# Kernel tuning notes

Measured on AMD Instinct MI355X. Metric: run time of the kernel, lower is better.

The kernel has to match this reference:

```python
import jax, jax.numpy as jnp
import numpy as np

B, S, D_IN, D_OUT = 4, 2048, 2048, 2048
E, R, TOP_K = 8, 8, 2
ALPHA = 16.0
SCALE = ALPHA / R  # alpha / r


def setup_inputs() -> dict:
    key = jax.random.key(0)
    ks = jax.random.split(key, 6)
    x = jax.random.normal(ks[0], (B, S, D_IN), dtype=jnp.float32)
    # base frozen linear: torch Linear weight [out, in], bias [out]
    W_base = jax.random.normal(ks[1], (D_OUT, D_IN), dtype=jnp.float32) / np.sqrt(D_IN)
    b_base = jax.random.normal(ks[2], (D_OUT,), dtype=jnp.float32) * 0.01
    # router: Linear(in_features, num_experts, bias=False) -> weight [E, in]
    W_router = jax.random.normal(ks[3], (E, D_IN), dtype=jnp.float32) / np.sqrt(D_IN)
    # LoRA experts: A [E, r, in], B [E, out, r] (torch inits B to zero; use small
    # random values so outputs/grads are non-trivial -- math is identical)
    A_w = jax.random.normal(ks[4], (E, R, D_IN), dtype=jnp.float32) / np.sqrt(D_IN)
    B_w = jax.random.normal(ks[5], (E, D_OUT, R), dtype=jnp.float32) * 0.02
    return {"x": x, "W_base": W_base, "b_base": b_base,
            "W_router": W_router, "A_w": A_w, "B_w": B_w}


def reference(x, W_base, b_base, W_router, A_w, B_w):
    # frozen base linear: [B,S,out]
    y = jnp.einsum('bsd,od->bso', x, W_base) + b_base
    # router: logits [B,S,E] -> top-k + softmax over the k selected logits
    logits = jnp.einsum('bsd,ed->bse', x, W_router)
    topk_vals, topk_idx = jax.lax.top_k(logits, TOP_K)       # [B,S,k]
    gates = jax.nn.softmax(topk_vals, axis=-1)               # [B,S,k]
    # all-experts LoRA compute (matches the original dense-stack semantics)
    h = jnp.einsum('bsd,erd->bser', x, A_w)                  # [B,S,E,r]
    expert_outs = jnp.einsum('bser,eor->bseo', h, B_w) * SCALE  # [B,S,E,out]
    # gather the top-k expert outputs and combine with gates
    topk_outs = jnp.take_along_axis(expert_outs, topk_idx[..., None], axis=2)  # [B,S,k,out]
    fused = jnp.sum(topk_outs * gates[..., None], axis=2)    # [B,S,out]
    return y + fused
```

## Files before the change

### kernel.cpp

```cpp
#include <hip/hip_runtime.h>

typedef unsigned short u16;
typedef __attribute__((ext_vector_type(8))) short short8;
typedef __attribute__((ext_vector_type(4))) float f32x4;

#define GLL16(g, l) __builtin_amdgcn_global_load_lds(                         \
    (const __attribute__((address_space(1))) void*)(g),                        \
    (__attribute__((address_space(3))) void*)(l), 16, 0, 0)

__device__ __forceinline__ u16 f2bf(float f) {
  union { float f; unsigned u; } v; v.f = f;
  unsigned u = v.u;
  return (u16)((u + 0x7FFFu + ((u >> 16) & 1u)) >> 16);
}

__device__ __forceinline__ float bf2f(u16 u) {
  union { unsigned u; float f; } v; v.u = ((unsigned)u) << 16;
  return v.f;
}

__device__ __forceinline__ ushort4 cvt4(float4 v) {
  ushort4 o; o.x = f2bf(v.x); o.y = f2bf(v.y); o.z = f2bf(v.z); o.w = f2bf(v.w);
  return o;
}

__global__ __launch_bounds__(512) void k_pre(
    const float* __restrict__ x, const float* __restrict__ Wr,
    const float* __restrict__ Wb, const float* __restrict__ Aw,
    const float* __restrict__ Bw,
    u16* __restrict__ xbf, float* __restrict__ logits,
    u16* __restrict__ wbf, u16* __restrict__ aabf, u16* __restrict__ bmt)
{
  __shared__ float wlds[16384];
  {
    const float4* src = (const float4*)Wr;
    float4* dst = (float4*)wlds;
    int t = threadIdx.x;
#pragma unroll
    for (int i = 0; i < 8; ++i) dst[t + i * 512] = src[t + i * 512];
  }
  __syncthreads();
  const int wave = threadIdx.x >> 6, lane = threadIdx.x & 63;
  const float4* wv = (const float4*)wlds;
#pragma unroll 1
  for (int s = 0; s < 2; ++s) {
    int tok = blockIdx.x * 16 + wave * 2 + s;
    const float4* xrow = (const float4*)(x + tok * 2048);
    ushort4* orow = (ushort4*)(xbf + tok * 2048);
    float acc[8];
#pragma unroll
    for (int e = 0; e < 8; ++e) acc[e] = 0.f;
#pragma unroll 1
    for (int i = 0; i < 8; ++i) {
      float4 xv = xrow[lane + i * 64];
      orow[lane + i * 64] = cvt4(xv);
#pragma unroll
      for (int e = 0; e < 8; ++e) {
        float4 b = wv[e * 512 + lane + i * 64];
        acc[e] += xv.x * b.x + xv.y * b.y + xv.z * b.z + xv.w * b.w;
      }
    }
#pragma unroll
    for (int e = 0; e < 8; ++e) {
      float v = acc[e];
#pragma unroll
      for (int off = 32; off > 0; off >>= 1) v += __shfl_xor(v, off, 64);
      acc[e] = v;
    }
    if (lane == 0) {
#pragma unroll
      for (int e = 0; e < 8; ++e) logits[tok * 8 + e] = acc[e];
    }
  }
  const int tidg = blockIdx.x * 512 + threadIdx.x;
  {
    const float4* src = (const float4*)Wb;
    ushort4* dst = (ushort4*)wbf;
#pragma unroll
    for (int i = 0; i < 4; ++i)
      dst[tidg + i * 262144] = cvt4(src[tidg + i * 262144]);
  }
  if (tidg < 32768) {
    ((ushort4*)aabf)[tidg] = cvt4(((const float4*)Aw)[tidg]);
  }
  if (tidg < 2048) {
    const int n = tidg;
#pragma unroll
    for (int e = 0; e < 8; ++e) {
      const float4* src = (const float4*)(Bw + e * 16384 + n * 8);
      ushort4* dst = (ushort4*)(bmt + n * 64 + e * 8);
      dst[0] = cvt4(src[0]);
      dst[1] = cvt4(src[1]);
    }
  }
}

__global__ __launch_bounds__(256) void k_hgemm(
    const u16* __restrict__ xbf, const u16* __restrict__ aabf,
    u16* __restrict__ P)
{
  __shared__ u16 As[256 * 64];
  __shared__ u16 Bs[64 * 64];
  int t = threadIdx.x, wave = t >> 6, lane = t & 63;
  int mBase = blockIdx.x * 256;
  int ks = blockIdx.y;
  int fr = lane & 15, fg = lane >> 4;
  int lrow = lane >> 3, lcol = (lane & 7) * 8;
  f32x4 zero = {0.f, 0.f, 0.f, 0.f};
  f32x4 acc[4][4];
#pragma unroll
  for (int i = 0; i < 4; ++i)
#pragma unroll
    for (int j = 0; j < 4; ++j) acc[i][j] = zero;
#pragma unroll 1
  for (int it = 0; it < 4; ++it) {
    int k0 = ks * 256 + it * 64;
    __syncthreads();
#pragma unroll
    for (int cc = 0; cc < 8; ++cc) {
      int c = wave * 8 + cc;
      GLL16(xbf + (mBase + c * 8 + lrow) * 2048 + k0 + lcol, &As[c * 512]);
    }
#pragma unroll
    for (int cc = 0; cc < 2; ++cc) {
      int c = wave * 2 + cc;
      GLL16(aabf + (c * 8 + lrow) * 2048 + k0 + lcol, &Bs[c * 512]);
    }
    __syncthreads();
#pragma unroll
    for (int kk = 0; kk < 2; ++kk) {
      short8 a[4], bfr[4];
#pragma unroll
      for (int i = 0; i < 4; ++i)
        a[i] = *(const short8*)&As[(wave * 64 + i * 16 + fr) * 64 + kk * 32 + fg * 8];
#pragma unroll
      for (int j = 0; j < 4; ++j)
        bfr[j] = *(const short8*)&Bs[(j * 16 + fr) * 64 + kk * 32 + fg * 8];
#pragma unroll
      for (int i = 0; i < 4; ++i)
#pragma unroll
        for (int j = 0; j < 4; ++j)
          acc[i][j] = __builtin_amdgcn_mfma_f32_16x16x32_bf16(a[i], bfr[j], acc[i][j], 0, 0, 0);
    }
  }
#pragma unroll
  for (int i = 0; i < 4; ++i)
#pragma unroll
    for (int j = 0; j < 4; ++j)
#pragma unroll
      for (int r = 0; r < 4; ++r) {
        int m = mBase + wave * 64 + i * 16 + fg * 4 + r;
        int n = j * 16 + fr;
        P[(ks * 8192 + m) * 64 + n] = f2bf(acc[i][j][r]);
      }
}

__global__ __launch_bounds__(256) void k_topk(
    const float* __restrict__ logits, const u16* __restrict__ P,
    u16* __restrict__ G)
{
  int t = threadIdx.x, wave = t >> 6, lane = t & 63;
  int tok = blockIdx.x * 4 + wave;
  const float* lg = logits + tok * 8;
  float la[8];
#pragma unroll
  for (int e = 0; e < 8; ++e) la[e] = lg[e];
  float v0 = la[0]; int i0 = 0;
#pragma unroll
  for (int e = 1; e < 8; ++e) { if (la[e] > v0) { v0 = la[e]; i0 = e; } }
  float v1 = -3.4e38f; int i1 = 0;
#pragma unroll
  for (int e = 0; e < 8; ++e) { if (e != i0 && la[e] > v1) { v1 = la[e]; i1 = e; } }
  float ex = expf(v1 - v0);
  float inv = 1.f / (1.f + ex);
  float gate0 = inv, gate1 = ex * inv;
  int e = lane >> 3;
  float h = 0.f;
#pragma unroll
  for (int ks = 0; ks < 8; ++ks) h += bf2f(P[(ks * 8192 + tok) * 64 + lane]);
  float g = (e == i0) ? gate0 : ((e == i1) ? gate1 : 0.f);
  G[tok * 64 + lane] = f2bf(2.0f * g * h);
}

__global__ __launch_bounds__(512, 2) void k_main(
    const u16* __restrict__ xbf, const u16* __restrict__ wbf,
    const u16* __restrict__ G, const u16* __restrict__ BmT,
    const float* __restrict__ bias, float* __restrict__ out)
{
  __shared__ u16 lds[65536];
  const int tid = threadIdx.x;
  const int w = tid >> 6, lane = tid & 63;
  const int fr = lane & 15, fg = lane >> 4;
  const int wr = w >> 2, wc = w & 3;

  const int b0 = blockIdx.x;
  const int wg = (b0 & 7) * 32 + (b0 >> 3);
  const int mBase = (wg >> 3) * 256;
  const int nBase = (wg & 7) * 256;

  const int rl = lane >> 3;
  const int ce = ((lane & 7) ^ rl) << 3;
  const int swz = (fr & 7) << 3;
  const int colk0 = (fg * 8) ^ swz;
  const int colk1 = (32 + fg * 8) ^ swz;
  const int aOff = (wr * 128 + fr) * 64;
  const int bOff = (wc * 64 + fr) * 64;

  const u16* pAlo = xbf + (mBase + w * 8 + rl) * 2048 + ce;
  const u16* pAhi = pAlo + 128 * 2048;
  const u16* pBlo = wbf + (nBase + w * 8 + rl) * 2048 + ce;
  const u16* pBhi = pBlo + 128 * 2048;

  f32x4 acc[8][4];
  const f32x4 zero = {0.f, 0.f, 0.f, 0.f};
#pragma unroll
  for (int mi = 0; mi < 8; ++mi)
#pragma unroll
    for (int nj = 0; nj < 4; ++nj) acc[mi][nj] = zero;

  short8 Aa[2][2], Ab[2][2];
  short8 Bx[4][2], By[4][2];

#define LGKM(N) asm volatile("s_waitcnt lgkmcnt(" #N ")" ::: "memory")
#define VMC(N)  asm volatile("s_waitcnt vmcnt(" #N ")" ::: "memory")
#define BAR()   __builtin_amdgcn_s_barrier()

#define SA_LO(OFF) { GLL16(pAlo, lds + (OFF) + w * 512);                      \
                     GLL16(pAlo + 131072, lds + (OFF) + 4096 + w * 512);      \
                     pAlo += 64; }
#define SA_HI(OFF) { GLL16(pAhi, lds + (OFF) + 8192 + w * 512);               \
                     GLL16(pAhi + 131072, lds + (OFF) + 12288 + w * 512);     \
                     pAhi += 64; }
#define SB_LO(OFF) { GLL16(pBlo, lds + 32768 + (OFF) + w * 512);              \
                     GLL16(pBlo + 131072, lds + 32768 + (OFF) + 4096 + w * 512); \
                     pBlo += 64; }
#define SB_HI(OFF) { GLL16(pBhi, lds + 32768 + (OFF) + 8192 + w * 512);       \
                     GLL16(pBhi + 131072, lds + 32768 + (OFF) + 12288 + w * 512); \
                     pBhi += 64; }

#define RDA(DST, BUF, MI0)                                                    \
  DST[0][0] = *(const short8*)((BUF) + aOff + (MI0) * 1024 + colk0);          \
  DST[0][1] = *(const short8*)((BUF) + aOff + (MI0) * 1024 + colk1);          \
  DST[1][0] = *(const short8*)((BUF) + aOff + ((MI0) + 1) * 1024 + colk0);    \
  DST[1][1] = *(const short8*)((BUF) + aOff + ((MI0) + 1) * 1024 + colk1);

#define RDB(DST, BUF, NJ0)                                                    \
  DST[(NJ0)][0] = *(const short8*)((BUF) + bOff + (NJ0) * 1024 + colk0);      \
  DST[(NJ0)][1] = *(const short8*)((BUF) + bOff + (NJ0) * 1024 + colk1);      \
  DST[(NJ0)+1][0] = *(const short8*)((BUF) + bOff + ((NJ0)+1) * 1024 + colk0);\
  DST[(NJ0)+1][1] = *(const short8*)((BUF) + bOff + ((NJ0)+1) * 1024 + colk1);

#define MFMA16(AV, BV, MI0)                                                   \
  __builtin_amdgcn_s_setprio(1);                                              \
  _Pragma("unroll")                                                           \
  for (int kk = 0; kk < 2; ++kk)                                              \
    _Pragma("unroll")                                                         \
    for (int q = 0; q < 2; ++q)                                               \
      _Pragma("unroll")                                                       \
      for (int nj = 0; nj < 4; ++nj)                                          \
        acc[(MI0) + q][nj] = __builtin_amdgcn_mfma_f32_16x16x32_bf16(         \
            AV[q][kk], BV[nj][kk], acc[(MI0) + q][nj], 0, 0, 0);              \
  __builtin_amdgcn_s_setprio(0);

#define TILE(P, BC, BN, SAL, SAH, SBL, SBH, VMCP2)                            \
  {                                                                           \
    const u16* Acur = lds + (P) * 16384;                                      \
    const u16* Anxt = lds + (1 - (P)) * 16384;                                \
    const u16* Bnxt = lds + 32768 + (1 - (P)) * 16384;                        \
                                                                      \
    SAL                                                                       \
    RDA(Ab, Acur, 2)                                                          \
    LGKM(4);                                                                  \
    MFMA16(Aa, BC, 0)                                                         \
    BAR();                                                                    \
                                                                      \
    SAH                                                                       \
    RDA(Aa, Acur, 4)                                                          \
    LGKM(4);                                                                  \
    MFMA16(Ab, BC, 2)                                                         \
    VMC(4);                                                                   \
    BAR();                                                                    \
                                                                      \
    SBL                                                                       \
    RDA(Ab, Acur, 6)                                                          \
    RDB(BN, Bnxt, 0)                                                          \
    LGKM(8);                                                                  \
    MFMA16(Aa, BC, 4)                                                         \
    VMCP2;                                                                    \
    BAR();                                                                    \
                                                                      \
    SBH                                                                       \
    RDA(Aa, Anxt, 0)                                                          \
    RDB(BN, Bnxt, 2)                                                          \
    LGKM(8);                                                                  \
    MFMA16(Ab, BC, 6)                                                         \
    BAR();                                                                    \
  }

  SA_LO(0) SA_HI(0)
  SB_LO(0) SB_HI(0)
  SB_LO(16384) SB_HI(16384)
  VMC(4);
  BAR();
  {
    const u16* Bb0 = lds + 32768;
    RDB(Bx, Bb0, 0)
    RDB(Bx, Bb0, 2)
    RDA(Aa, lds, 0)
  }

#pragma unroll 1
  for (int tt = 0; tt < 15; ++tt) {
    TILE(0, Bx, By, SA_LO(16384), SA_HI(16384), SB_LO(0), SB_HI(0), VMC(2))
    TILE(1, By, Bx, SA_LO(0), SA_HI(0), SB_LO(16384), SB_HI(16384), VMC(2))
  }

  {
    const u16* pTlo = BmT + (nBase + w * 8 + rl) * 64 + ce;
    const u16* pThi = pTlo + 128 * 64;
    TILE(0, Bx, By, SA_LO(16384), SA_HI(16384),
         { GLL16(pTlo, lds + 32768 + w * 512);
           GLL16(pTlo + 4096, lds + 32768 + 4096 + w * 512); },
         { GLL16(pThi, lds + 32768 + 8192 + w * 512);
           GLL16(pThi + 4096, lds + 32768 + 12288 + w * 512); },
         VMC(2))
  }
  {
    const u16* pGlo = G + (mBase + w * 8 + rl) * 64 + ce;
    const u16* pGhi = pGlo + 128 * 64;
    TILE(1, By, Bx,
         { GLL16(pGlo, lds + w * 512);
           GLL16(pGlo + 4096, lds + 4096 + w * 512); },
         { GLL16(pGhi, lds + 8192 + w * 512);
           GLL16(pGhi + 4096, lds + 12288 + w * 512); },
         { }, { }, VMC(0))
  }

  {
    const u16* Acur = lds;
    RDA(Ab, Acur, 2)
    LGKM(4);
    MFMA16(Aa, Bx, 0)
    RDA(Aa, Acur, 4)
    LGKM(4);
    MFMA16(Ab, Bx, 2)
    RDA(Ab, Acur, 6)
    LGKM(4);
    MFMA16(Aa, Bx, 4)
    LGKM(0);
    MFMA16(Ab, Bx, 6)
  }

#pragma unroll
  for (int nj = 0; nj < 4; ++nj) {
    const int n = nBase + wc * 64 + nj * 16 + fr;
    const float bv = bias[n];
#pragma unroll
    for (int mi = 0; mi < 8; ++mi) {
      const int m = mBase + wr * 128 + mi * 16 + fg * 4;
#pragma unroll
      for (int r = 0; r < 4; ++r)
        out[(m + r) * 2048 + n] = acc[mi][nj][r] + bv;
    }
  }
#undef TILE
#undef MFMA16
#undef RDB
#undef RDA
#undef SB_HI
#undef SB_LO
#undef SA_HI
#undef SA_LO
#undef BAR
#undef VMC
#undef LGKM
}

extern "C" void kernel_launch(void* const* d_in, const int* in_sizes, int n_in,
                              void* d_out, int out_size, void* d_ws, size_t ws_size,
                              hipStream_t stream) {
  const float* x  = (const float*)d_in[0];
  const float* Wb = (const float*)d_in[1];
  const float* bb = (const float*)d_in[2];
  const float* Wr = (const float*)d_in[3];
  const float* Aw = (const float*)d_in[4];
  const float* Bw = (const float*)d_in[5];

  char* ws = (char*)d_ws;
  u16*   xbf  = (u16*)  (ws + 0);
  u16*   wbf  = (u16*)  (ws + 33554432);
  u16*   aabf = (u16*)  (ws + 41943040);
  u16*   bmt  = (u16*)  (ws + 42205184);
  float* lgt  = (float*)(ws + 42467328);
  u16*   G    = (u16*)  (ws + 42729472);
  u16*   P   = (u16*)d_out;
  float* out = (float*)d_out;

  hipLaunchKernelGGL(k_pre,   dim3(512),   dim3(512), 0, stream,
                     x, Wr, Wb, Aw, Bw, xbf, lgt, wbf, aabf, bmt);
  hipLaunchKernelGGL(k_hgemm, dim3(32, 8), dim3(256), 0, stream, xbf, aabf, P);
  hipLaunchKernelGGL(k_topk,  dim3(2048),  dim3(256), 0, stream, lgt, P, G);
  hipLaunchKernelGGL(k_main,  dim3(256),   dim3(512), 0, stream,
                     xbf, wbf, G, bmt, bb, out);
}
```

Baseline: 111.1 us.

## Fuse top-k gating into LoRA-A GEMM via last-block atomic counter

Removes the separate top-k/gate kernel launch. Each M-tile of the split-K h-GEMM increments an atomic counter, and the last of its 8 K-split blocks reduces the partial products, computes top-2 softmax gates and writes G. This saves one kernel launch and its launch gap. In exchange it adds threadfences, an atomic per block and serialized tail work on 32 blocks.

```diff
diff --git a/kernel.cpp b/kernel.cpp
--- a/kernel.cpp
+++ b/kernel.cpp
@@ -29,8 +29,10 @@
     const float* __restrict__ Wb, const float* __restrict__ Aw,
     const float* __restrict__ Bw,
     u16* __restrict__ xbf, float* __restrict__ logits,
-    u16* __restrict__ wbf, u16* __restrict__ aabf, u16* __restrict__ bmt)
+    u16* __restrict__ wbf, u16* __restrict__ aabf, u16* __restrict__ bmt,
+    unsigned* __restrict__ cnt)
 {
+  if (blockIdx.x == 0 && threadIdx.x < 32) cnt[threadIdx.x] = 0;
   __shared__ float wlds[16384];
   {
     const float4* src = (const float4*)Wr;
@@ -95,14 +97,16 @@
   }
 }
 
-__global__ __launch_bounds__(256) void k_hgemm(
+__global__ __launch_bounds__(256) void k_hg(
     const u16* __restrict__ xbf, const u16* __restrict__ aabf,
-    u16* __restrict__ P)
+    const float* __restrict__ logits,
+    u16* __restrict__ P, u16* __restrict__ G, unsigned* __restrict__ cnt)
 {
   __shared__ u16 As[256 * 64];
   __shared__ u16 Bs[64 * 64];
   int t = threadIdx.x, wave = t >> 6, lane = t & 63;
-  int mBase = blockIdx.x * 256;
+  int mtile = blockIdx.x;
+  int mBase = mtile * 256;
   int ks = blockIdx.y;
   int fr = lane & 15, fg = lane >> 4;
   int lrow = lane >> 3, lcol = (lane & 7) * 8;
@@ -153,33 +157,46 @@
         int n = j * 16 + fr;
         P[(ks * 8192 + m) * 64 + n] = f2bf(acc[i][j][r]);
       }
-}
-
-__global__ __launch_bounds__(256) void k_topk(
-    const float* __restrict__ logits, const u16* __restrict__ P,
-    u16* __restrict__ G)
-{
-  int t = threadIdx.x, wave = t >> 6, lane = t & 63;
-  int tok = blockIdx.x * 4 + wave;
-  const float* lg = logits + tok * 8;
-  float la[8];
-#pragma unroll
-  for (int e = 0; e < 8; ++e) la[e] = lg[e];
-  float v0 = la[0]; int i0 = 0;
-#pragma unroll
-  for (int e = 1; e < 8; ++e) { if (la[e] > v0) { v0 = la[e]; i0 = e; } }
-  float v1 = -3.4e38f; int i1 = 0;
-#pragma unroll
-  for (int e = 0; e < 8; ++e) { if (e != i0 && la[e] > v1) { v1 = la[e]; i1 = e; } }
-  float ex = expf(v1 - v0);
-  float inv = 1.f / (1.f + ex);
-  float gate0 = inv, gate1 = ex * inv;
-  int e = lane >> 3;
-  float h = 0.f;
-#pragma unroll
-  for (int ks = 0; ks < 8; ++ks) h += bf2f(P[(ks * 8192 + tok) * 64 + lane]);
-  float g = (e == i0) ? gate0 : ((e == i1) ? gate1 : 0.f);
-  G[tok * 64 + lane] = f2bf(2.0f * g * h);
+
+  __threadfence();
+  __syncthreads();
+  __shared__ unsigned oldc;
+  if (t == 0) oldc = atomicAdd(&cnt[mtile], 1u);
+  __syncthreads();
+  if (oldc != 7u) return;
+  __threadfence();
+
+  float* g0s = (float*)As;
+  float* g1s = g0s + 256;
+  int*   i0s = (int*)(g1s + 256);
+  int*   i1s = i0s + 256;
+  {
+    const float* lg = logits + (mBase + t) * 8;
+    float la[8];
+#pragma unroll
+    for (int e = 0; e < 8; ++e) la[e] = lg[e];
+    float v0 = la[0]; int i0 = 0;
+#pragma unroll
+    for (int e = 1; e < 8; ++e) { if (la[e] > v0) { v0 = la[e]; i0 = e; } }
+    float v1 = -3.4e38f; int i1 = 0;
+#pragma unroll
+    for (int e = 0; e < 8; ++e) { if (e != i0 && la[e] > v1) { v1 = la[e]; i1 = e; } }
+    float ex = expf(v1 - v0);
+    float inv = 1.f / (1.f + ex);
+    g0s[t] = inv; g1s[t] = ex * inv; i0s[t] = i0; i1s[t] = i1;
+  }
+  __syncthreads();
+#pragma unroll 1
+  for (int i = 0; i < 64; ++i) {
+    const int idx = i * 256 + t;
+    const int trel = idx >> 6, er = idx & 63, e = er >> 3;
+    float h = 0.f;
+#pragma unroll
+    for (int k2 = 0; k2 < 8; ++k2) h += bf2f(P[k2 * 524288 + mBase * 64 + idx]);
+    const float g = (e == i0s[trel]) ? g0s[trel]
+                  : ((e == i1s[trel]) ? g1s[trel] : 0.f);
+    G[mBase * 64 + idx] = f2bf(2.0f * g * h);
+  }
 }
 
 __global__ __launch_bounds__(512, 2) void k_main(
@@ -387,19 +404,20 @@
   const float* Bw = (const float*)d_in[5];
 
   char* ws = (char*)d_ws;
-  u16*   xbf  = (u16*)  (ws + 0);
-  u16*   wbf  = (u16*)  (ws + 33554432);
-  u16*   aabf = (u16*)  (ws + 41943040);
-  u16*   bmt  = (u16*)  (ws + 42205184);
-  float* lgt  = (float*)(ws + 42467328);
-  u16*   G    = (u16*)  (ws + 42729472);
+  u16*      xbf  = (u16*)     (ws + 0);
+  u16*      wbf  = (u16*)     (ws + 33554432);
+  u16*      aabf = (u16*)     (ws + 41943040);
+  u16*      bmt  = (u16*)     (ws + 42205184);
+  float*    lgt  = (float*)   (ws + 42467328);
+  u16*      G    = (u16*)     (ws + 42729472);
+  unsigned* cnt  = (unsigned*)(ws + 43778048);
   u16*   P   = (u16*)d_out;
   float* out = (float*)d_out;
 
-  hipLaunchKernelGGL(k_pre,   dim3(512),   dim3(512), 0, stream,
-                     x, Wr, Wb, Aw, Bw, xbf, lgt, wbf, aabf, bmt);
-  hipLaunchKernelGGL(k_hgemm, dim3(32, 8), dim3(256), 0, stream, xbf, aabf, P);
-  hipLaunchKernelGGL(k_topk,  dim3(2048),  dim3(256), 0, stream, lgt, P, G);
-  hipLaunchKernelGGL(k_main,  dim3(256),   dim3(512), 0, stream,
+  hipLaunchKernelGGL(k_pre,  dim3(512),   dim3(512), 0, stream,
+                     x, Wr, Wb, Aw, Bw, xbf, lgt, wbf, aabf, bmt, cnt);
+  hipLaunchKernelGGL(k_hg,   dim3(32, 8), dim3(256), 0, stream,
+                     xbf, aabf, lgt, P, G, cnt);
+  hipLaunchKernelGGL(k_main, dim3(256),   dim3(512), 0, stream,
                      xbf, wbf, G, bmt, bb, out);
 }
```

Result: slower. 164.2 us (+47.8%).

## Retile main GEMM to 128x256 blocks with 4 waves and single-buffered A

Applied to the files above, without the earlier changes.

The main fused GEMM moves from 256x256 output tiles with 8 waves to 128x256 tiles with 4 waves and 512 blocks. Each wave now computes 64x128, and B is double-buffered while A uses a single LDS buffer, so LDS use drops to 80 KB. The aim is better CU coverage (512 blocks across 256 CUs) and higher occupancy. In exchange, arithmetic intensity per block falls, every k-step now waits on a full vmcnt(0) barrier, and the overlap of global loads with MFMA is reduced.

```diff
diff --git a/kernel.cpp b/kernel.cpp
--- a/kernel.cpp
+++ b/kernel.cpp
@@ -182,195 +182,161 @@
   G[tok * 64 + lane] = f2bf(2.0f * g * h);
 }
 
-__global__ __launch_bounds__(512, 2) void k_main(
+__global__ __launch_bounds__(256, 2) void k_main(
     const u16* __restrict__ xbf, const u16* __restrict__ wbf,
     const u16* __restrict__ G, const u16* __restrict__ BmT,
     const float* __restrict__ bias, float* __restrict__ out)
 {
-  __shared__ u16 lds[65536];
+  __shared__ u16 lds[40960];
   const int tid = threadIdx.x;
   const int w = tid >> 6, lane = tid & 63;
   const int fr = lane & 15, fg = lane >> 4;
-  const int wr = w >> 2, wc = w & 3;
+  const int wr = w >> 1, wc = w & 1;
 
   const int b0 = blockIdx.x;
-  const int wg = (b0 & 7) * 32 + (b0 >> 3);
-  const int mBase = (wg >> 3) * 256;
-  const int nBase = (wg & 7) * 256;
+  const int xcd = b0 & 7, i = b0 >> 3;
+  const int mBase = (xcd * 8 + (i >> 3)) * 128;
+  const int nBase = (i & 7) * 256;
 
   const int rl = lane >> 3;
   const int ce = ((lane & 7) ^ rl) << 3;
   const int swz = (fr & 7) << 3;
   const int colk0 = (fg * 8) ^ swz;
   const int colk1 = (32 + fg * 8) ^ swz;
-  const int aOff = (wr * 128 + fr) * 64;
-  const int bOff = (wc * 64 + fr) * 64;
-
-  const u16* pAlo = xbf + (mBase + w * 8 + rl) * 2048 + ce;
-  const u16* pAhi = pAlo + 128 * 2048;
-  const u16* pBlo = wbf + (nBase + w * 8 + rl) * 2048 + ce;
-  const u16* pBhi = pBlo + 128 * 2048;
-
-  f32x4 acc[8][4];
+  const int aOff = (wr * 64 + fr) * 64;
+  const int bOff = (wc * 128 + fr) * 64;
+
+  const u16* pA = xbf + (mBase + w * 8 + rl) * 2048 + ce;
+  const u16* pB = wbf + (nBase + w * 8 + rl) * 2048 + ce;
+
+  f32x4 acc[4][8];
   const f32x4 zero = {0.f, 0.f, 0.f, 0.f};
 #pragma unroll
-  for (int mi = 0; mi < 8; ++mi)
-#pragma unroll
-    for (int nj = 0; nj < 4; ++nj) acc[mi][nj] = zero;
-
-  short8 Aa[2][2], Ab[2][2];
-  short8 Bx[4][2], By[4][2];
+  for (int mi = 0; mi < 4; ++mi)
+#pragma unroll
+    for (int nj = 0; nj < 8; ++nj) acc[mi][nj] = zero;
+
+  short8 a[4][2];
+  short8 U[2][2], V[2][2];
 
 #define LGKM(N) asm volatile("s_waitcnt lgkmcnt(" #N ")" ::: "memory")
 #define VMC(N)  asm volatile("s_waitcnt vmcnt(" #N ")" ::: "memory")
 #define BAR()   __builtin_amdgcn_s_barrier()
 
-#define SA_LO(OFF) { GLL16(pAlo, lds + (OFF) + w * 512);                      \
-                     GLL16(pAlo + 131072, lds + (OFF) + 4096 + w * 512);      \
-                     pAlo += 64; }
-#define SA_HI(OFF) { GLL16(pAhi, lds + (OFF) + 8192 + w * 512);               \
-                     GLL16(pAhi + 131072, lds + (OFF) + 12288 + w * 512);     \
-                     pAhi += 64; }
-#define SB_LO(OFF) { GLL16(pBlo, lds + 32768 + (OFF) + w * 512);              \
-                     GLL16(pBlo + 131072, lds + 32768 + (OFF) + 4096 + w * 512); \
-                     pBlo += 64; }
-#define SB_HI(OFF) { GLL16(pBhi, lds + 32768 + (OFF) + 8192 + w * 512);       \
-                     GLL16(pBhi + 131072, lds + 32768 + (OFF) + 12288 + w * 512); \
-                     pBhi += 64; }
-
-#define RDA(DST, BUF, MI0)                                                    \
-  DST[0][0] = *(const short8*)((BUF) + aOff + (MI0) * 1024 + colk0);          \
-  DST[0][1] = *(const short8*)((BUF) + aOff + (MI0) * 1024 + colk1);          \
-  DST[1][0] = *(const short8*)((BUF) + aOff + ((MI0) + 1) * 1024 + colk0);    \
-  DST[1][1] = *(const short8*)((BUF) + aOff + ((MI0) + 1) * 1024 + colk1);
-
-#define RDB(DST, BUF, NJ0)                                                    \
-  DST[(NJ0)][0] = *(const short8*)((BUF) + bOff + (NJ0) * 1024 + colk0);      \
-  DST[(NJ0)][1] = *(const short8*)((BUF) + bOff + (NJ0) * 1024 + colk1);      \
-  DST[(NJ0)+1][0] = *(const short8*)((BUF) + bOff + ((NJ0)+1) * 1024 + colk0);\
-  DST[(NJ0)+1][1] = *(const short8*)((BUF) + bOff + ((NJ0)+1) * 1024 + colk1);
-
-#define MFMA16(AV, BV, MI0)                                                   \
+#define SA() { GLL16(pA,          lds + w * 512);                             \
+               GLL16(pA + 65536,  lds + 2048 + w * 512);                      \
+               GLL16(pA + 131072, lds + 4096 + w * 512);                      \
+               GLL16(pA + 196608, lds + 6144 + w * 512);                      \
+               pA += 64; }
+#define SB_LO(BOFF) { GLL16(pB,          lds + (BOFF) + w * 512);             \
+                      GLL16(pB + 65536,  lds + (BOFF) + 2048 + w * 512);      \
+                      GLL16(pB + 131072, lds + (BOFF) + 4096 + w * 512);      \
+                      GLL16(pB + 196608, lds + (BOFF) + 6144 + w * 512); }
+#define SB_HI(BOFF) { GLL16(pB + 262144, lds + (BOFF) + 8192 + w * 512);      \
+                      GLL16(pB + 327680, lds + (BOFF) + 10240 + w * 512);     \
+                      GLL16(pB + 393216, lds + (BOFF) + 12288 + w * 512);     \
+                      GLL16(pB + 458752, lds + (BOFF) + 14336 + w * 512);     \
+                      pB += 64; }
+
+#define RDA()                                                                 \
+  _Pragma("unroll")                                                           \
+  for (int mi = 0; mi < 4; ++mi) {                                            \
+    a[mi][0] = *(const short8*)(lds + aOff + mi * 1024 + colk0);              \
+    a[mi][1] = *(const short8*)(lds + aOff + mi * 1024 + colk1);              \
+  }
+
+#define RDB2(DST, BOFF, NJ0)                                                  \
+  DST[0][0] = *(const short8*)(lds + (BOFF) + bOff + (NJ0) * 1024 + colk0);   \
+  DST[0][1] = *(const short8*)(lds + (BOFF) + bOff + (NJ0) * 1024 + colk1);   \
+  DST[1][0] = *(const short8*)(lds + (BOFF) + bOff + ((NJ0)+1) * 1024 + colk0);\
+  DST[1][1] = *(const short8*)(lds + (BOFF) + bOff + ((NJ0)+1) * 1024 + colk1);
+
+#define MFMAP(BV, NJ0)                                                        \
   __builtin_amdgcn_s_setprio(1);                                              \
   _Pragma("unroll")                                                           \
   for (int kk = 0; kk < 2; ++kk)                                              \
     _Pragma("unroll")                                                         \
-    for (int q = 0; q < 2; ++q)                                               \
+    for (int mi = 0; mi < 4; ++mi)                                            \
       _Pragma("unroll")                                                       \
-      for (int nj = 0; nj < 4; ++nj)                                          \
-        acc[(MI0) + q][nj] = __builtin_amdgcn_mfma_f32_16x16x32_bf16(         \
-            AV[q][kk], BV[nj][kk], acc[(MI0) + q][nj], 0, 0, 0);              \
+      for (int j = 0; j < 2; ++j)                                             \
+        acc[mi][(NJ0) + j] = __builtin_amdgcn_mfma_f32_16x16x32_bf16(         \
+            a[mi][kk], BV[j][kk], acc[mi][(NJ0) + j], 0, 0, 0);               \
   __builtin_amdgcn_s_setprio(0);
 
-#define TILE(P, BC, BN, SAL, SAH, SBL, SBH, VMCP2)                            \
+#define TILE(BCUR, BNXT, SA_STMT, SBL_STMT, SBH_STMT)                         \
   {                                                                           \
-    const u16* Acur = lds + (P) * 16384;                                      \
-    const u16* Anxt = lds + (1 - (P)) * 16384;                                \
-    const u16* Bnxt = lds + 32768 + (1 - (P)) * 16384;                        \
                                                                       \
-    SAL                                                                       \
-    RDA(Ab, Acur, 2)                                                          \
+    VMC(0);                                                                   \
+    BAR();                                                                    \
+    RDB2(U, BCUR, 0)                                                          \
+    RDA()                                                                     \
+    RDB2(V, BCUR, 2)                                                          \
     LGKM(4);                                                                  \
-    MFMA16(Aa, BC, 0)                                                         \
+    MFMAP(U, 0)                                                               \
     BAR();                                                                    \
                                                                       \
-    SAH                                                                       \
-    RDA(Aa, Acur, 4)                                                          \
+    SA_STMT                                                                   \
+    RDB2(U, BCUR, 4)                                                          \
     LGKM(4);                                                                  \
-    MFMA16(Ab, BC, 2)                                                         \
-    VMC(4);                                                                   \
-    BAR();                                                                    \
+    MFMAP(V, 2)                                                               \
                                                                       \
-    SBL                                                                       \
-    RDA(Ab, Acur, 6)                                                          \
-    RDB(BN, Bnxt, 0)                                                          \
-    LGKM(8);                                                                  \
-    MFMA16(Aa, BC, 4)                                                         \
-    VMCP2;                                                                    \
-    BAR();                                                                    \
+    SBL_STMT                                                                  \
+    RDB2(V, BCUR, 6)                                                          \
+    LGKM(4);                                                                  \
+    MFMAP(U, 4)                                                               \
                                                                       \
-    SBH                                                                       \
-    RDA(Aa, Anxt, 0)                                                          \
-    RDB(BN, Bnxt, 2)                                                          \
-    LGKM(8);                                                                  \
-    MFMA16(Ab, BC, 6)                                                         \
-    BAR();                                                                    \
-  }
-
-  SA_LO(0) SA_HI(0)
-  SB_LO(0) SB_HI(0)
-  SB_LO(16384) SB_HI(16384)
-  VMC(4);
-  BAR();
-  {
-    const u16* Bb0 = lds + 32768;
-    RDB(Bx, Bb0, 0)
-    RDB(Bx, Bb0, 2)
-    RDA(Aa, lds, 0)
-  }
+    SBH_STMT                                                                  \
+    LGKM(0);                                                                  \
+    MFMAP(V, 6)                                                               \
+  }
+
+  SA()
+  SB_LO(8192) SB_HI(8192)
 
 #pragma unroll 1
   for (int tt = 0; tt < 15; ++tt) {
-    TILE(0, Bx, By, SA_LO(16384), SA_HI(16384), SB_LO(0), SB_HI(0), VMC(2))
-    TILE(1, By, Bx, SA_LO(0), SA_HI(0), SB_LO(16384), SB_HI(16384), VMC(2))
-  }
-
+    TILE(8192, 24576, SA(), SB_LO(24576), SB_HI(24576))
+    TILE(24576, 8192, SA(), SB_LO(8192), SB_HI(8192))
+  }
+  TILE(8192, 24576, SA(), SB_LO(24576), SB_HI(24576))
   {
-    const u16* pTlo = BmT + (nBase + w * 8 + rl) * 64 + ce;
-    const u16* pThi = pTlo + 128 * 64;
-    TILE(0, Bx, By, SA_LO(16384), SA_HI(16384),
-         { GLL16(pTlo, lds + 32768 + w * 512);
-           GLL16(pTlo + 4096, lds + 32768 + 4096 + w * 512); },
-         { GLL16(pThi, lds + 32768 + 8192 + w * 512);
-           GLL16(pThi + 4096, lds + 32768 + 12288 + w * 512); },
-         VMC(2))
-  }
-  {
-    const u16* pGlo = G + (mBase + w * 8 + rl) * 64 + ce;
-    const u16* pGhi = pGlo + 128 * 64;
-    TILE(1, By, Bx,
-         { GLL16(pGlo, lds + w * 512);
-           GLL16(pGlo + 4096, lds + 4096 + w * 512); },
-         { GLL16(pGhi, lds + 8192 + w * 512);
-           GLL16(pGhi + 4096, lds + 12288 + w * 512); },
-         { }, { }, VMC(0))
-  }
-
-  {
-    const u16* Acur = lds;
-    RDA(Ab, Acur, 2)
-    LGKM(4);
-    MFMA16(Aa, Bx, 0)
-    RDA(Aa, Acur, 4)
-    LGKM(4);
-    MFMA16(Ab, Bx, 2)
-    RDA(Ab, Acur, 6)
-    LGKM(4);
-    MFMA16(Aa, Bx, 4)
-    LGKM(0);
-    MFMA16(Ab, Bx, 6)
-  }
-
-#pragma unroll
-  for (int nj = 0; nj < 4; ++nj) {
-    const int n = nBase + wc * 64 + nj * 16 + fr;
+    const u16* pG = G + (mBase + w * 8 + rl) * 64 + ce;
+    const u16* pT = BmT + (nBase + w * 8 + rl) * 64 + ce;
+    TILE(24576, 8192,
+         { GLL16(pG,        lds + w * 512);
+           GLL16(pG + 2048, lds + 2048 + w * 512);
+           GLL16(pG + 4096, lds + 4096 + w * 512);
+           GLL16(pG + 6144, lds + 6144 + w * 512); },
+         { GLL16(pT,        lds + 8192 + w * 512);
+           GLL16(pT + 2048, lds + 8192 + 2048 + w * 512);
+           GLL16(pT + 4096, lds + 8192 + 4096 + w * 512);
+           GLL16(pT + 6144, lds + 8192 + 6144 + w * 512); },
+         { GLL16(pT + 8192,  lds + 8192 + 8192 + w * 512);
+           GLL16(pT + 10240, lds + 8192 + 10240 + w * 512);
+           GLL16(pT + 12288, lds + 8192 + 12288 + w * 512);
+           GLL16(pT + 14336, lds + 8192 + 14336 + w * 512); })
+  }
+  TILE(8192, 24576, {}, {}, {})
+
+#pragma unroll
+  for (int nj = 0; nj < 8; ++nj) {
+    const int n = nBase + wc * 128 + nj * 16 + fr;
     const float bv = bias[n];
 #pragma unroll
-    for (int mi = 0; mi < 8; ++mi) {
-      const int m = mBase + wr * 128 + mi * 16 + fg * 4;
+    for (int mi = 0; mi < 4; ++mi) {
+      const int m = mBase + wr * 64 + mi * 16 + fg * 4;
 #pragma unroll
       for (int r = 0; r < 4; ++r)
         out[(m + r) * 2048 + n] = acc[mi][nj][r] + bv;
     }
   }
 #undef TILE
-#undef MFMA16
-#undef RDB
+#undef MFMAP
+#undef RDB2
 #undef RDA
 #undef SB_HI
 #undef SB_LO
-#undef SA_HI
-#undef SA_LO
+#undef SA
 #undef BAR
 #undef VMC
 #undef LGKM
@@ -400,6 +366,6 @@
                      x, Wr, Wb, Aw, Bw, xbf, lgt, wbf, aabf, bmt);
   hipLaunchKernelGGL(k_hgemm, dim3(32, 8), dim3(256), 0, stream, xbf, aabf, P);
   hipLaunchKernelGGL(k_topk,  dim3(2048),  dim3(256), 0, stream, lgt, P, G);
-  hipLaunchKernelGGL(k_main,  dim3(256),   dim3(512), 0, stream,
+  hipLaunchKernelGGL(k_main,  dim3(512),   dim3(256), 0, stream,
                      xbf, wbf, G, bmt, bb, out);
 }
```

Measured after the change: 108.9 us. 2.0% less time.
